# Optimization experiments

Measured on AMD Instinct MI355X. Metric: run time of the kernel, lower is better.

The kernel has to match this reference:

```python
import jax, jax.numpy as jnp
import numpy as np

N_NODES = 100000


def gcn_conv(x, src, dst, W, b, n):
    # x: [N, F_in]; src/dst: [E+N] (self-loops already appended)
    h = x @ W  # [N, F_out]
    deg = jax.ops.segment_sum(jnp.ones_like(dst, dtype=h.dtype), dst, num_segments=n)
    dinv = jnp.where(deg > 0, jax.lax.rsqrt(deg), 0.0)
    norm = dinv[src] * dinv[dst]  # [E+N]
    msgs = h[src] * norm[:, None]  # gather + scale
    out = jax.ops.segment_sum(msgs, dst, num_segments=n)  # scatter-add at dst
    return out + b


def setup_inputs() -> dict:
    key = jax.random.key(0)
    k1, k2, k3, ke = jax.random.split(key, 4)
    d = 64
    x = jax.random.normal(k1, (N_NODES, d), dtype=jnp.float32)
    edge_index = jax.random.randint(ke, (2, 1000000), 0, N_NODES, dtype=jnp.int64)
    s = 1.0 / np.sqrt(d)
    W1 = jax.random.normal(k2, (d, d), dtype=jnp.float32) * s
    b1 = jnp.zeros((d,), dtype=jnp.float32)
    W2 = jax.random.normal(k3, (d, d), dtype=jnp.float32) * s
    b2 = jnp.zeros((d,), dtype=jnp.float32)
    return {"x": x, "edge_index": edge_index, "W1": W1, "b1": b1, "W2": W2, "b2": b2}


def reference(x, edge_index, W1, b1, W2, b2):
    n = x.shape[0]
    loops = jnp.arange(n, dtype=edge_index.dtype)
    src = jnp.concatenate([edge_index[0], loops])
    dst = jnp.concatenate([edge_index[1], loops])
    h = gcn_conv(x, src, dst, W1, b1, n)
    h = jax.nn.relu(h)
    out = gcn_conv(h, src, dst, W2, b2, n)
    return out
```

## Files before the change

### kernel.cpp

```cpp
#include <hip/hip_runtime.h>

#define F 64
#define NCH 64

typedef __attribute__((ext_vector_type(8))) short bf16x8;
typedef __attribute__((ext_vector_type(4))) float f32x4;

static __device__ __forceinline__ unsigned short f2bf(float f) {
    unsigned u = __float_as_uint(f);
    return (unsigned short)((u + 0x7fffu + ((u >> 16) & 1u)) >> 16);
}
static __device__ __forceinline__ float bflo(unsigned u) { return __uint_as_float(u << 16); }
static __device__ __forceinline__ float bfhi(unsigned u) { return __uint_as_float(u & 0xffff0000u); }

__global__ __launch_bounds__(256) void k_hist(const int* __restrict__ dst,
                                              int* __restrict__ histM,
                                              int E, int chunk, int NB) {
    extern __shared__ int h[];
    const int t = threadIdx.x;
    for (int i = t; i < NB; i += 256) h[i] = 0;
    __syncthreads();
    const int lo = blockIdx.x * chunk;
    const int hi = min(E, lo + chunk);
    for (int e = lo + t; e < hi; e += 256) {
        atomicAdd(&h[dst[e] >> 8], 1);
    }
    __syncthreads();
    for (int i = t; i < NB; i += 256) histM[i * NCH + blockIdx.x] = h[i];
}

__global__ __launch_bounds__(256) void s_part(const int* __restrict__ v,
                                              int* __restrict__ part, int M) {
    __shared__ int sd[256];
    const int t = threadIdx.x;
    const int base = blockIdx.x * 1024 + t * 4;
    int4 d = *(const int4*)&v[base];
    sd[t] = d.x + d.y + d.z + d.w;
    __syncthreads();
    for (int off = 128; off > 0; off >>= 1) {
        if (t < off) sd[t] += sd[t + off];
        __syncthreads();
    }
    if (t == 0) part[blockIdx.x] = sd[0];
}

__global__ __launch_bounds__(256) void s_scanp(int* __restrict__ part, int nb) {
    __shared__ int sums[256];
    const int t = threadIdx.x;
    int s = (t < nb) ? part[t] : 0;
    sums[t] = s;
    __syncthreads();
    for (int off = 1; off < 256; off <<= 1) {
        int v = (t >= off) ? sums[t - off] : 0;
        __syncthreads();
        sums[t] += v;
        __syncthreads();
    }
    if (t < nb) part[t] = sums[t] - s;
}

__global__ __launch_bounds__(256) void s_emit(int* __restrict__ v,
                                              const int* __restrict__ part, int M) {
    __shared__ int sums[256];
    const int t = threadIdx.x;
    const int base = blockIdx.x * 1024 + t * 4;
    int4 d = *(const int4*)&v[base];
    int tot = d.x + d.y + d.z + d.w;
    sums[t] = tot;
    __syncthreads();
    for (int off = 1; off < 256; off <<= 1) {
        int x = (t >= off) ? sums[t - off] : 0;
        __syncthreads();
        sums[t] += x;
        __syncthreads();
    }
    int o0 = part[blockIdx.x] + sums[t] - tot;
    int4 o;
    o.x = o0; o.y = o0 + d.x; o.z = o.y + d.y; o.w = o.z + d.z;
    *(int4*)&v[base] = o;
}

__global__ __launch_bounds__(256) void k_scatter2(const int* __restrict__ src,
                                                  const int* __restrict__ dst,
                                                  const int* __restrict__ scanM,
                                                  int* __restrict__ ebuf,
                                                  int E, int chunk, int NB) {
    extern __shared__ int cur[];
    const int t = threadIdx.x;
    for (int i = t; i < NB; i += 256) cur[i] = scanM[i * NCH + blockIdx.x];
    __syncthreads();
    const int lo = blockIdx.x * chunk;
    const int hi = min(E, lo + chunk);
    for (int e = lo + t; e < hi; e += 256) {
        int s = src[e];
        int d = dst[e];
        int p = atomicAdd(&cur[d >> 8], 1);
        ebuf[p] = s | ((d & 255) << 17);
    }
}

__global__ __launch_bounds__(256) void k_csr(const int* __restrict__ ebuf,
                                             const int* __restrict__ scanM,
                                             int* __restrict__ rowptr,
                                             int* __restrict__ csr,
                                             float* __restrict__ dinv,
                                             int N, int E, int NB) {
    __shared__ int hist[256];
    __shared__ int scn[256];
    __shared__ int cur[256];
    const int t = threadIdx.x;
    const int bkt = blockIdx.x;
    const int beg = scanM[bkt * NCH];
    const int end = (bkt + 1 < NB) ? scanM[(bkt + 1) * NCH] : E;

    hist[t] = 0;
    __syncthreads();
    for (int e = beg + t; e < end; e += 256)
        atomicAdd(&hist[((unsigned)ebuf[e]) >> 17], 1);
    __syncthreads();

    scn[t] = hist[t];
    __syncthreads();
    for (int off = 1; off < 256; off <<= 1) {
        int v = (t >= off) ? scn[t - off] : 0;
        __syncthreads();
        scn[t] += v;
        __syncthreads();
    }

    {
        int excl = scn[t] - hist[t];
        int rp = beg + excl;
        int node = (bkt << 8) + t;
        cur[t] = rp;
        if (node < N) {
            rowptr[node] = rp;
            dinv[node] = rsqrtf((float)(hist[t] + 1));
        }
    }
    if (bkt == NB - 1 && t == 0) rowptr[N] = E;
    __syncthreads();

    for (int e = beg + t; e < end; e += 256) {
        int pk = ebuf[e];
        int p = atomicAdd(&cur[((unsigned)pk) >> 17], 1);
        csr[p] = pk & 0x1FFFF;
    }
}

__global__ __launch_bounds__(256) void k_gemm_mfma(const float* __restrict__ X,
                                                   const float* __restrict__ W,
                                                   const float* __restrict__ dinv,
                                                   unsigned short* __restrict__ hs, int N) {
    __shared__ unsigned short Wt[64 * 72];
    __shared__ unsigned short Xs[64 * 72];
    const int t = threadIdx.x;
    const int row0 = blockIdx.x * 64;

#pragma unroll
    for (int i = 0; i < 16; ++i) {
        int e = t + i * 256;
        int k = e >> 6, n = e & 63;
        Wt[n * 72 + k] = f2bf(W[e]);
    }
#pragma unroll
    for (int i = 0; i < 4; ++i) {
        int idx = t + i * 256;
        int r = idx >> 4, c = (idx & 15) * 4;
        int gr = row0 + r;
        float4 v = make_float4(0.f, 0.f, 0.f, 0.f);
        if (gr < N) v = *(const float4*)&X[(size_t)gr * F + c];
        unsigned p0 = (unsigned)f2bf(v.x) | ((unsigned)f2bf(v.y) << 16);
        unsigned p1 = (unsigned)f2bf(v.z) | ((unsigned)f2bf(v.w) << 16);
        *(uint2*)&Xs[r * 72 + c] = make_uint2(p0, p1);
    }
    __syncthreads();

    const int w    = t >> 6;
    const int lane = t & 63;
    const int l15  = lane & 15;
    const int quad = lane >> 4;

    bf16x8 bf[4][2];
#pragma unroll
    for (int ct = 0; ct < 4; ++ct)
#pragma unroll
        for (int kc = 0; kc < 2; ++kc)
            bf[ct][kc] = *(const bf16x8*)&Wt[(ct * 16 + l15) * 72 + kc * 32 + quad * 8];

    const int am = w * 16 + l15;
    bf16x8 af0 = *(const bf16x8*)&Xs[am * 72 + quad * 8];
    bf16x8 af1 = *(const bf16x8*)&Xs[am * 72 + 32 + quad * 8];

    f32x4 acc[4];
#pragma unroll
    for (int ct = 0; ct < 4; ++ct) {
        f32x4 z = {0.f, 0.f, 0.f, 0.f};
        z = __builtin_amdgcn_mfma_f32_16x16x32_bf16(af0, bf[ct][0], z, 0, 0, 0);
        z = __builtin_amdgcn_mfma_f32_16x16x32_bf16(af1, bf[ct][1], z, 0, 0, 0);
        acc[ct] = z;
    }

    float dv[4];
#pragma unroll
    for (int r = 0; r < 4; ++r) {
        int row = row0 + w * 16 + quad * 4 + r;
        dv[r] = (row < N) ? dinv[row] : 0.f;
    }
#pragma unroll
    for (int ct = 0; ct < 4; ++ct) {
#pragma unroll
        for (int r = 0; r < 4; ++r) {
            int row = row0 + w * 16 + quad * 4 + r;
            if (row < N)
                hs[(size_t)row * F + ct * 16 + l15] = f2bf(acc[ct][r] * dv[r]);
        }
    }
}

__global__ __launch_bounds__(256) void k_agg(const unsigned short* __restrict__ hs,
                                             const int* __restrict__ rowptr,
                                             const int* __restrict__ csr,
                                             const float* __restrict__ dinv,
                                             const float* __restrict__ b,
                                             float* __restrict__ out,
                                             int N, int do_relu) {
    int gid = blockIdx.x * 256 + threadIdx.x;
    int node = gid >> 3;
    int lane = gid & 7;
    if (node >= N) return;
    int beg = rowptr[node];
    int end = rowptr[node + 1];
    const int q = lane * 8;
    const uint4* hsb = (const uint4*)hs;

    float acc0, acc1, acc2, acc3, acc4, acc5, acc6, acc7;
    {
        uint4 u = hsb[(size_t)node * 8 + lane];
        acc0 = bflo(u.x); acc1 = bfhi(u.x);
        acc2 = bflo(u.y); acc3 = bfhi(u.y);
        acc4 = bflo(u.z); acc5 = bfhi(u.z);
        acc6 = bflo(u.w); acc7 = bfhi(u.w);
    }

    for (int base = beg; base < end; base += 16) {
        int i0 = base + lane;
        int i1 = base + 8 + lane;
        int x0 = (i0 < end) ? csr[i0] : 0;
        int x1 = (i1 < end) ? csr[i1] : 0;
        uint4 r[16];
#pragma unroll
        for (int k = 0; k < 8; ++k) {
            int s = __shfl(x0, k, 8);
            r[k] = hsb[(size_t)s * 8 + lane];
        }
#pragma unroll
        for (int k = 0; k < 8; ++k) {
            int s = __shfl(x1, k, 8);
            r[8 + k] = hsb[(size_t)s * 8 + lane];
        }
        int cnt = min(16, end - base);
#pragma unroll
        for (int k = 0; k < 16; ++k) {
            if (k < cnt) {
                uint4 u = r[k];
                acc0 += bflo(u.x); acc1 += bfhi(u.x);
                acc2 += bflo(u.y); acc3 += bfhi(u.y);
                acc4 += bflo(u.z); acc5 += bfhi(u.z);
                acc6 += bflo(u.w); acc7 += bfhi(u.w);
            }
        }
    }

    float sc = dinv[node];
    float4 b0 = *(const float4*)&b[q];
    float4 b1 = *(const float4*)&b[q + 4];
    float4 o0 = make_float4(acc0 * sc + b0.x, acc1 * sc + b0.y,
                            acc2 * sc + b0.z, acc3 * sc + b0.w);
    float4 o1 = make_float4(acc4 * sc + b1.x, acc5 * sc + b1.y,
                            acc6 * sc + b1.z, acc7 * sc + b1.w);
    if (do_relu) {
        o0.x = fmaxf(o0.x, 0.f); o0.y = fmaxf(o0.y, 0.f);
        o0.z = fmaxf(o0.z, 0.f); o0.w = fmaxf(o0.w, 0.f);
        o1.x = fmaxf(o1.x, 0.f); o1.y = fmaxf(o1.y, 0.f);
        o1.z = fmaxf(o1.z, 0.f); o1.w = fmaxf(o1.w, 0.f);
    }
    *(float4*)&out[(size_t)node * F + q] = o0;
    *(float4*)&out[(size_t)node * F + q + 4] = o1;
}

extern "C" void kernel_launch(void* const* d_in, const int* in_sizes, int n_in,
                              void* d_out, int out_size, void* d_ws, size_t ws_size,
                              hipStream_t stream) {
    const float* x  = (const float*)d_in[0];
    const int*   ei = (const int*)d_in[1];
    const float* W1 = (const float*)d_in[2];
    const float* b1 = (const float*)d_in[3];
    const float* W2 = (const float*)d_in[4];
    const float* b2 = (const float*)d_in[5];
    float* out = (float*)d_out;

    const int N = in_sizes[0] / F;
    const int E = in_sizes[1] / 2;
    const int* src = ei;
    const int* dst = ei + E;

    const int NB = (N + 255) >> 8;
    const int chunk = (E + NCH - 1) / NCH;
    const int M  = NB * NCH;
    const int Mp = ((M + 1023) / 1024) * 1024;
    const int nb2 = Mp / 1024;

    char* ws = (char*)d_ws;
    size_t a = 0;
    float* dinv   = (float*)(ws + a); a += ((size_t)N * 4 + 255) & ~(size_t)255;
    int*   part2  = (int*)(ws + a);   a += ((size_t)nb2 * 4 + 255) & ~(size_t)255;
    int*   rowptr = (int*)(ws + a);   a += ((size_t)(N + 1) * 4 + 255) & ~(size_t)255;
    int*   histM  = (int*)(ws + a);   a += ((size_t)Mp * 4 + 255) & ~(size_t)255;
    int*   ebuf   = (int*)(ws + a);   a += ((size_t)E * 4 + 255) & ~(size_t)255;
    int*   csr    = (int*)(ws + a);   a += ((size_t)E * 4 + 255) & ~(size_t)255;
    unsigned short* hs = (unsigned short*)(ws + a);

    const size_t ldsNB = (size_t)NB * 4;
    const int gGemm = (N + 63) / 64;
    const int gAgg  = (int)(((long long)N * 8 + 255) / 256);

    hipMemsetAsync(histM, 0, (size_t)Mp * 4, stream);
    k_hist<<<NCH, 256, ldsNB, stream>>>(dst, histM, E, chunk, NB);
    s_part<<<nb2, 256, 0, stream>>>(histM, part2, Mp);
    s_scanp<<<1, 256, 0, stream>>>(part2, nb2);
    s_emit<<<nb2, 256, 0, stream>>>(histM, part2, Mp);
    k_scatter2<<<NCH, 256, ldsNB, stream>>>(src, dst, histM, ebuf, E, chunk, NB);
    k_csr<<<NB, 256, 0, stream>>>(ebuf, histM, rowptr, csr, dinv, N, E, NB);

    k_gemm_mfma<<<gGemm, 256, 0, stream>>>(x, W1, dinv, hs, N);
    k_agg<<<gAgg, 256, 0, stream>>>(hs, rowptr, csr, dinv, b1, out, N, 1);

    k_gemm_mfma<<<gGemm, 256, 0, stream>>>(out, W2, dinv, hs, N);
    k_agg<<<gAgg, 256, 0, stream>>>(hs, rowptr, csr, dinv, b2, out, N, 0);
}
```

Before: 205.9 us.

## Fuse layer-1 aggregation with layer-2 GEMM and pretranspose weights to bf16

Adds a small prep kernel that converts and transposes W1 and W2 to bf16 once, so the GEMM blocks load them with vector copies instead of scattered converted stores. A new kernel aggregates layer 1 (bias, ReLU) for 256 nodes into LDS as bf16, then runs the layer-2 MFMA GEMM on that tile directly and writes the scaled hs2. This removes the fp32 round trip of the hidden activations through global memory and one kernel launch. In exchange the fused kernel uses large LDS and 512 threads, which may lower occupancy for the latency-bound gather phase, and it rounds the intermediate activations to bf16 as the old GEMM already did.

```diff
diff --git a/kernel.cpp b/kernel.cpp
--- a/kernel.cpp
+++ b/kernel.cpp
@@ -12,6 +12,21 @@
 }
 static __device__ __forceinline__ float bflo(unsigned u) { return __uint_as_float(u << 16); }
 static __device__ __forceinline__ float bfhi(unsigned u) { return __uint_as_float(u & 0xffff0000u); }
+
+__global__ __launch_bounds__(256) void k_prep(const float* __restrict__ W1,
+                                              const float* __restrict__ W2,
+                                              unsigned short* __restrict__ W1t,
+                                              unsigned short* __restrict__ W2t) {
+    const float* W = blockIdx.x ? W2 : W1;
+    unsigned short* Wt = blockIdx.x ? W2t : W1t;
+    const int t = threadIdx.x;
+#pragma unroll
+    for (int i = 0; i < 16; ++i) {
+        int e = t + i * 256;
+        int n = e >> 6, k = e & 63;
+        Wt[e] = f2bf(W[k * 64 + n]);
+    }
+}
 
 __global__ __launch_bounds__(256) void k_hist(const int* __restrict__ dst,
                                               int* __restrict__ histM,
@@ -148,20 +163,20 @@
     }
 }
 
-__global__ __launch_bounds__(256) void k_gemm_mfma(const float* __restrict__ X,
-                                                   const float* __restrict__ W,
-                                                   const float* __restrict__ dinv,
-                                                   unsigned short* __restrict__ hs, int N) {
-    __shared__ unsigned short Wt[64 * 72];
+__global__ __launch_bounds__(256) void k_gemm1(const float* __restrict__ X,
+                                               const unsigned short* __restrict__ W1t,
+                                               const float* __restrict__ dinv,
+                                               unsigned short* __restrict__ hs, int N) {
+    __shared__ unsigned short Wl[64 * 72];
     __shared__ unsigned short Xs[64 * 72];
     const int t = threadIdx.x;
     const int row0 = blockIdx.x * 64;
 
 #pragma unroll
-    for (int i = 0; i < 16; ++i) {
-        int e = t + i * 256;
-        int k = e >> 6, n = e & 63;
-        Wt[n * 72 + k] = f2bf(W[e]);
+    for (int i = 0; i < 2; ++i) {
+        int idx = t + i * 256;
+        int n = idx >> 3, k = (idx & 7) * 8;
+        *(uint4*)&Wl[n * 72 + k] = ((const uint4*)W1t)[idx];
     }
 #pragma unroll
     for (int i = 0; i < 4; ++i) {
@@ -186,7 +201,7 @@
     for (int ct = 0; ct < 4; ++ct)
 #pragma unroll
         for (int kc = 0; kc < 2; ++kc)
-            bf[ct][kc] = *(const bf16x8*)&Wt[(ct * 16 + l15) * 72 + kc * 32 + quad * 8];
+            bf[ct][kc] = *(const bf16x8*)&Wl[(ct * 16 + l15) * 72 + kc * 32 + quad * 8];
 
     const int am = w * 16 + l15;
     bf16x8 af0 = *(const bf16x8*)&Xs[am * 72 + quad * 8];
@@ -218,13 +233,129 @@
     }
 }
 
+__global__ __launch_bounds__(512) void k_aggmm(const unsigned short* __restrict__ hs1,
+                                               const int* __restrict__ rowptr,
+                                               const int* __restrict__ csr,
+                                               const unsigned short* __restrict__ W2t,
+                                               const float* __restrict__ b1,
+                                               unsigned short* __restrict__ hs2, int N) {
+    __shared__ unsigned short Act[256 * 72];
+    __shared__ unsigned short Wl[64 * 72];
+    __shared__ float sdv[256];
+    const int t = threadIdx.x;
+    const int node0 = blockIdx.x << 8;
+
+    if (t < 512) {
+        int idx = t;
+        int n = idx >> 3, k = (idx & 7) * 8;
+        *(uint4*)&Wl[n * 72 + k] = ((const uint4*)W2t)[idx];
+    }
+
+    const int lane = t & 7;
+    const int nsub = t >> 3;
+    const uint4* hsb = (const uint4*)hs1;
+    float4 bb0 = *(const float4*)&b1[lane * 8];
+    float4 bb1 = *(const float4*)&b1[lane * 8 + 4];
+
+#pragma unroll
+    for (int it = 0; it < 4; ++it) {
+        int local = it * 64 + nsub;
+        int node = node0 + local;
+        float sc = 0.f;
+        unsigned p0 = 0, p1 = 0, p2 = 0, p3 = 0;
+        if (node < N) {
+            int beg = rowptr[node];
+            int end = rowptr[node + 1];
+            sc = rsqrtf((float)(end - beg + 1));
+            float a0, a1, a2, a3, a4, a5, a6, a7;
+            {
+                uint4 u = hsb[(size_t)node * 8 + lane];
+                a0 = bflo(u.x); a1 = bfhi(u.x);
+                a2 = bflo(u.y); a3 = bfhi(u.y);
+                a4 = bflo(u.z); a5 = bfhi(u.z);
+                a6 = bflo(u.w); a7 = bfhi(u.w);
+            }
+            for (int base = beg; base < end; base += 16) {
+                int i0 = base + lane;
+                int i1 = base + 8 + lane;
+                int x0 = (i0 < end) ? csr[i0] : 0;
+                int x1 = (i1 < end) ? csr[i1] : 0;
+                uint4 r[16];
+#pragma unroll
+                for (int k = 0; k < 8; ++k) {
+                    int s = __shfl(x0, k, 8);
+                    r[k] = hsb[(size_t)s * 8 + lane];
+                }
+#pragma unroll
+                for (int k = 0; k < 8; ++k) {
+                    int s = __shfl(x1, k, 8);
+                    r[8 + k] = hsb[(size_t)s * 8 + lane];
+                }
+                int cnt = min(16, end - base);
+#pragma unroll
+                for (int k = 0; k < 16; ++k) {
+                    if (k < cnt) {
+                        uint4 u = r[k];
+                        a0 += bflo(u.x); a1 += bfhi(u.x);
+                        a2 += bflo(u.y); a3 += bfhi(u.y);
+                        a4 += bflo(u.z); a5 += bfhi(u.z);
+                        a6 += bflo(u.w); a7 += bfhi(u.w);
+                    }
+                }
+            }
+            float o0 = fmaxf(a0 * sc + bb0.x, 0.f), o1 = fmaxf(a1 * sc + bb0.y, 0.f);
+            float o2 = fmaxf(a2 * sc + bb0.z, 0.f), o3 = fmaxf(a3 * sc + bb0.w, 0.f);
+            float o4 = fmaxf(a4 * sc + bb1.x, 0.f), o5 = fmaxf(a5 * sc + bb1.y, 0.f);
+            float o6 = fmaxf(a6 * sc + bb1.z, 0.f), o7 = fmaxf(a7 * sc + bb1.w, 0.f);
+            p0 = (unsigned)f2bf(o0) | ((unsigned)f2bf(o1) << 16);
+            p1 = (unsigned)f2bf(o2) | ((unsigned)f2bf(o3) << 16);
+            p2 = (unsigned)f2bf(o4) | ((unsigned)f2bf(o5) << 16);
+            p3 = (unsigned)f2bf(o6) | ((unsigned)f2bf(o7) << 16);
+        }
+        *(uint4*)&Act[local * 72 + lane * 8] = make_uint4(p0, p1, p2, p3);
+        if (lane == 0) sdv[local] = sc;
+    }
+    __syncthreads();
+
+    const int w    = t >> 6;
+    const int l    = t & 63;
+    const int l15  = l & 15;
+    const int quad = l >> 4;
+
+    bf16x8 bf[4][2];
+#pragma unroll
+    for (int nt = 0; nt < 4; ++nt)
+#pragma unroll
+        for (int kc = 0; kc < 2; ++kc)
+            bf[nt][kc] = *(const bf16x8*)&Wl[(nt * 16 + l15) * 72 + kc * 32 + quad * 8];
+
+#pragma unroll
+    for (int mt = 0; mt < 2; ++mt) {
+        int m0 = w * 32 + mt * 16;
+        bf16x8 af0 = *(const bf16x8*)&Act[(m0 + l15) * 72 + quad * 8];
+        bf16x8 af1 = *(const bf16x8*)&Act[(m0 + l15) * 72 + 32 + quad * 8];
+#pragma unroll
+        for (int nt = 0; nt < 4; ++nt) {
+            f32x4 z = {0.f, 0.f, 0.f, 0.f};
+            z = __builtin_amdgcn_mfma_f32_16x16x32_bf16(af0, bf[nt][0], z, 0, 0, 0);
+            z = __builtin_amdgcn_mfma_f32_16x16x32_bf16(af1, bf[nt][1], z, 0, 0, 0);
+#pragma unroll
+            for (int r = 0; r < 4; ++r) {
+                int row = m0 + quad * 4 + r;
+                int node = node0 + row;
+                if (node < N)
+                    hs2[(size_t)node * F + nt * 16 + l15] = f2bf(z[r] * sdv[row]);
+            }
+        }
+    }
+}
+
 __global__ __launch_bounds__(256) void k_agg(const unsigned short* __restrict__ hs,
                                              const int* __restrict__ rowptr,
                                              const int* __restrict__ csr,
                                              const float* __restrict__ dinv,
                                              const float* __restrict__ b,
-                                             float* __restrict__ out,
-                                             int N, int do_relu) {
+                                             float* __restrict__ out, int N) {
     int gid = blockIdx.x * 256 + threadIdx.x;
     int node = gid >> 3;
     int lane = gid & 7;
@@ -242,7 +373,6 @@
         acc4 = bflo(u.z); acc5 = bfhi(u.z);
         acc6 = bflo(u.w); acc7 = bfhi(u.w);
     }
-
     for (int base = beg; base < end; base += 16) {
         int i0 = base + lane;
         int i1 = base + 8 + lane;
@@ -279,12 +409,6 @@
                             acc2 * sc + b0.z, acc3 * sc + b0.w);
     float4 o1 = make_float4(acc4 * sc + b1.x, acc5 * sc + b1.y,
                             acc6 * sc + b1.z, acc7 * sc + b1.w);
-    if (do_relu) {
-        o0.x = fmaxf(o0.x, 0.f); o0.y = fmaxf(o0.y, 0.f);
-        o0.z = fmaxf(o0.z, 0.f); o0.w = fmaxf(o0.w, 0.f);
-        o1.x = fmaxf(o1.x, 0.f); o1.y = fmaxf(o1.y, 0.f);
-        o1.z = fmaxf(o1.z, 0.f); o1.w = fmaxf(o1.w, 0.f);
-    }
     *(float4*)&out[(size_t)node * F + q] = o0;
     *(float4*)&out[(size_t)node * F + q + 4] = o1;
 }
@@ -313,18 +437,22 @@
 
     char* ws = (char*)d_ws;
     size_t a = 0;
+    unsigned short* W1t = (unsigned short*)(ws + a); a += (4096 * 2 + 255) & ~(size_t)255;
+    unsigned short* W2t = (unsigned short*)(ws + a); a += (4096 * 2 + 255) & ~(size_t)255;
     float* dinv   = (float*)(ws + a); a += ((size_t)N * 4 + 255) & ~(size_t)255;
     int*   part2  = (int*)(ws + a);   a += ((size_t)nb2 * 4 + 255) & ~(size_t)255;
     int*   rowptr = (int*)(ws + a);   a += ((size_t)(N + 1) * 4 + 255) & ~(size_t)255;
     int*   histM  = (int*)(ws + a);   a += ((size_t)Mp * 4 + 255) & ~(size_t)255;
     int*   ebuf   = (int*)(ws + a);   a += ((size_t)E * 4 + 255) & ~(size_t)255;
     int*   csr    = (int*)(ws + a);   a += ((size_t)E * 4 + 255) & ~(size_t)255;
-    unsigned short* hs = (unsigned short*)(ws + a);
+    unsigned short* hs1 = (unsigned short*)(ws + a); a += ((size_t)N * F * 2 + 255) & ~(size_t)255;
+    unsigned short* hs2 = (unsigned short*)(ws + a);
 
     const size_t ldsNB = (size_t)NB * 4;
     const int gGemm = (N + 63) / 64;
     const int gAgg  = (int)(((long long)N * 8 + 255) / 256);
 
+    k_prep<<<2, 256, 0, stream>>>(W1, W2, W1t, W2t);
     hipMemsetAsync(histM, 0, (size_t)Mp * 4, stream);
     k_hist<<<NCH, 256, ldsNB, stream>>>(dst, histM, E, chunk, NB);
     s_part<<<nb2, 256, 0, stream>>>(histM, part2, Mp);
@@ -333,9 +461,7 @@
     k_scatter2<<<NCH, 256, ldsNB, stream>>>(src, dst, histM, ebuf, E, chunk, NB);
     k_csr<<<NB, 256, 0, stream>>>(ebuf, histM, rowptr, csr, dinv, N, E, NB);
 
-    k_gemm_mfma<<<gGemm, 256, 0, stream>>>(x, W1, dinv, hs, N);
-    k_agg<<<gAgg, 256, 0, stream>>>(hs, rowptr, csr, dinv, b1, out, N, 1);
-
-    k_gemm_mfma<<<gGemm, 256, 0, stream>>>(out, W2, dinv, hs, N);
-    k_agg<<<gAgg, 256, 0, stream>>>(hs, rowptr, csr, dinv, b2, out, N, 0);
-}
+    k_gemm1<<<gGemm, 256, 0, stream>>>(x, W1t, dinv, hs1, N);
+    k_aggmm<<<NB, 512, 0, stream>>>(hs1, rowptr, csr, W2t, b1, hs2, N);
+    k_agg<<<gAgg, 256, 0, stream>>>(hs2, rowptr, csr, dinv, b2, out, N);
+}
```

Result: faster. 198.3 us (-3.7%).
